# Kernel optimization log

Measured on AMD Instinct MI355X. Metric: run time of the kernel, lower is better.

The kernel has to match this reference:

```python
import jax, jax.numpy as jnp
import numpy as np

MAX_DISPARITY = 192


def _cost_volume(L, R, D):
    """Banded stereo correlation.

    cost[n, j, h, x] = sum_c L[n,c,h,x] * R[n,c,h,x-j], zero when x < j.
    Equivalent to the original full (W,W) matmul followed by per-disparity
    diagonal extraction + left zero-pad, but computed as D shifted
    dot-products (honors the banded structure).
    """
    N, C, H, W = L.shape
    Rp = jnp.pad(R, ((0, 0), (0, 0), (0, 0), (D - 1, 0)))  # left zero-pad

    def step(_, j):
        Rs = jax.lax.dynamic_slice_in_dim(Rp, D - 1 - j, W, axis=3)  # R shifted right by j
        c = jnp.einsum('nchw,nchw->nhw', L, Rs)
        return None, c

    _, cv = jax.lax.scan(step, None, jnp.arange(D))  # (D, N, H, W)
    return jnp.transpose(cv, (1, 0, 2, 3))  # (N, D, H, W)


def setup_inputs() -> dict:
    key = jax.random.key(0)
    ks = jax.random.split(key, 6)
    shapes = [(1, 32, 256, 512), (1, 32, 128, 256), (1, 32, 64, 128)]
    inp = {}
    for i, s in enumerate(shapes):
        inp[f'left{i}'] = jax.random.normal(ks[2 * i], s, dtype=jnp.float32)
        inp[f'right{i}'] = jax.random.normal(ks[2 * i + 1], s, dtype=jnp.float32)
    return inp


def reference(left0, right0, left1, right1, left2, right2):
    lefts = [left0, left1, left2]
    rights = [right0, right1, right2]
    max_disparity = min(MAX_DISPARITY, lefts[0].shape[-1])
    cost_volumes = []
    for i, (L, R) in enumerate(zip(lefts, rights)):
        D = max_disparity // (2 ** i)
        cost_volumes.append(_cost_volume(L, R, D))
    return tuple(cost_volumes)
```

## Files before the change

kernel.cpp:

```cpp
#include <hip/hip_runtime.h>


#define TX 128
#define TJ 192
#define JT 24
#define NCS 8
#define NSTG 4
#define LSW 128
#define RSW 320

#define NBLK_TOTAL 1344

typedef float vf4 __attribute__((ext_vector_type(4)));

__device__ __forceinline__ void gload_lds16(const float* g, float* l)
{
    __builtin_amdgcn_global_load_lds(
        (const __attribute__((address_space(1))) void*)g,
        (__attribute__((address_space(3))) void*)l,
        16, 0, 0);
}

__global__ __launch_bounds__(256, 3)
void cost_volume_fused(const float* __restrict__ L0, const float* __restrict__ R0,
                       const float* __restrict__ L1, const float* __restrict__ R1,
                       const float* __restrict__ L2, const float* __restrict__ R2,
                       float* __restrict__ out)
{
    __shared__ float Ls[2][NCS * LSW];
    __shared__ float Rs[2][NCS * RSW];

    const int id = blockIdx.x;
    const float* L; const float* R; float* o;
    int H, W, D, bx, h;
    if (id < 1024) {
        L = L0; R = R0; o = out;
        H = 256; W = 512; D = 192;
        bx = id & 3; h = id >> 2;
    } else if (id < 1280) {
        int r = id - 1024;
        L = L1; R = R1; o = out + (size_t)192 * 256 * 512;
        H = 128; W = 256; D = 96;
        bx = r & 1; h = r >> 1;
    } else {
        int r = id - 1280;
        L = L2; R = R2; o = out + (size_t)192 * 256 * 512 + (size_t)96 * 128 * 256;
        H = 64; W = 128; D = 48;
        bx = 0; h = r;
    }

    const int x0 = bx * TX;
    const int t  = threadIdx.x;
    const int tx = t & 31;
    const int ty = t >> 5;
    const int jbase = ty * JT;
    const int xg = x0 + 4 * tx;

    const size_t HW = (size_t)H * W;
    const float* Lb = L + (size_t)h * W;
    const float* Rb = R + (size_t)h * W;

    const bool active = (jbase < D);
    const bool live   = active && (xg + 3 >= jbase);

    float acc[JT][4];
    #pragma unroll
    for (int jj = 0; jj < JT; ++jj) {
        acc[jj][0] = 0.f; acc[jj][1] = 0.f; acc[jj][2] = 0.f; acc[jj][3] = 0.f;
    }

    const int rbase = 4 * tx - JT * ty + (TJ - 24);

    auto stage = [&](int c0, int p) {
        {
            int c = t >> 5, q = t & 31;
            gload_lds16(Lb + (size_t)(c0 + c) * HW + x0 + 4 * q, &Ls[p][4 * t]);
        }
        #pragma unroll
        for (int k = 0; k < 3; ++k) {
            int f = t + k * 256;
            if (f < NCS * 80) {
                int c = f / 80, q = f - 80 * c;
                int g = x0 - TJ + 4 * q;
                if (g < 0) g = 0;
                gload_lds16(Rb + (size_t)(c0 + c) * HW + g, &Rs[p][4 * f]);
            }
        }
    };

    stage(0, 0);
    __syncthreads();

    #pragma unroll
    for (int s = 0; s < NSTG; ++s) {
        if (s + 1 < NSTG) stage((s + 1) * NCS, (s + 1) & 1);
        if (live) {
            const float* Lsb = Ls[s & 1];
            const float* Rsb = Rs[s & 1];
            #pragma unroll 1
            for (int c = 0; c < NCS; ++c) {
                const float* Lc = Lsb + c * LSW;
                const float* Rc = Rsb + c * RSW + rbase;
                float lv[4], rw[28];
                *(vf4*)&lv[0] = *(const vf4*)(Lc + 4 * tx);
                #pragma unroll
                for (int k = 0; k < 7; ++k)
                    *(vf4*)&rw[4 * k] = *(const vf4*)(Rc + 4 * k);
                #pragma unroll
                for (int jj = 0; jj < JT; ++jj)
                    #pragma unroll
                    for (int i = 0; i < 4; ++i)
                        acc[jj][i] = fmaf(lv[i], rw[24 + i - jj], acc[jj][i]);
            }
        }
        if (s + 1 < NSTG) __syncthreads();
    }

    if (active) {
        #pragma unroll
        for (int jj = 0; jj < JT; ++jj) {
            int j = jbase + jj;
            float* p = o + ((size_t)j * H + h) * W + xg;
            vf4 v;
            #pragma unroll
            for (int i = 0; i < 4; ++i)
                v[i] = (xg + i >= j) ? acc[jj][i] : 0.f;
            __builtin_nontemporal_store(v, (vf4*)p);
        }
    }
}

extern "C" void kernel_launch(void* const* d_in, const int* in_sizes, int n_in,
                              void* d_out, int out_size, void* d_ws, size_t ws_size,
                              hipStream_t stream)
{
    const float* L0 = (const float*)d_in[0];
    const float* R0 = (const float*)d_in[1];
    const float* L1 = (const float*)d_in[2];
    const float* R1 = (const float*)d_in[3];
    const float* L2 = (const float*)d_in[4];
    const float* R2 = (const float*)d_in[5];
    float* out = (float*)d_out;

    cost_volume_fused<<<dim3(NBLK_TOTAL), dim3(256), 0, stream>>>(
        L0, R0, L1, R1, L2, R2, out);
}
```

Measured before the change: 173.1 us.

## Compute banded correlation with fp16 MFMA tiles and LDS diagonal extraction

```diff
diff --git a/kernel.cpp b/kernel.cpp
--- a/kernel.cpp
+++ b/kernel.cpp
@@ -1,25 +1,12 @@
 #include <hip/hip_runtime.h>
 
-
-#define TX 128
-#define TJ 192
-#define JT 24
-#define NCS 8
-#define NSTG 4
-#define LSW 128
-#define RSW 320
 
 #define NBLK_TOTAL 1344
 
 typedef float vf4 __attribute__((ext_vector_type(4)));
-
-__device__ __forceinline__ void gload_lds16(const float* g, float* l)
-{
-    __builtin_amdgcn_global_load_lds(
-        (const __attribute__((address_space(1))) void*)g,
-        (__attribute__((address_space(3))) void*)l,
-        16, 0, 0);
-}
+typedef float f32x4 __attribute__((ext_vector_type(4)));
+typedef _Float16 h4 __attribute__((ext_vector_type(4)));
+typedef _Float16 h8 __attribute__((ext_vector_type(8)));
 
 __global__ __launch_bounds__(256, 3)
 void cost_volume_fused(const float* __restrict__ L0, const float* __restrict__ R0,
@@ -27,8 +14,8 @@
                        const float* __restrict__ L2, const float* __restrict__ R2,
                        float* __restrict__ out)
 {
-    __shared__ float Ls[2][NCS * LSW];
-    __shared__ float Rs[2][NCS * RSW];
+    __shared__ __align__(16) unsigned short St[448 * 32];
+    __shared__ __align__(16) float Ep[4 * 1024];
 
     const int id = blockIdx.x;
     const float* L; const float* R; float* o;
@@ -49,83 +36,125 @@
         bx = 0; h = r;
     }
 
-    const int x0 = bx * TX;
+    const int x0 = bx * 128;
     const int t  = threadIdx.x;
-    const int tx = t & 31;
-    const int ty = t >> 5;
-    const int jbase = ty * JT;
-    const int xg = x0 + 4 * tx;
+    const int l  = t & 63;
+    const int w_ = t >> 6;
 
     const size_t HW = (size_t)H * W;
     const float* Lb = L + (size_t)h * W;
     const float* Rb = R + (size_t)h * W;
 
-    const bool active = (jbase < D);
-    const bool live   = active && (xg + 3 >= jbase);
+    char* Sb = (char*)St;
 
-    float acc[JT][4];
+    {
+        const int c0 = (t >> 5) * 4;
+        const int x4 = t & 31;
+        const float* gp = Lb + (size_t)c0 * HW + x0 + 4 * x4;
+        vf4 v0 = *(const vf4*)(gp);
+        vf4 v1 = *(const vf4*)(gp + HW);
+        vf4 v2 = *(const vf4*)(gp + 2 * HW);
+        vf4 v3 = *(const vf4*)(gp + 3 * HW);
+        #pragma unroll
+        for (int xi = 0; xi < 4; ++xi) {
+            int row = 4 * x4 + xi;
+            h4 hv = { (_Float16)v0[xi], (_Float16)v1[xi],
+                      (_Float16)v2[xi], (_Float16)v3[xi] };
+            *(h4*)(Sb + row * 64 + ((((c0 >> 3) ^ ((row >> 1) & 3)) << 4)
+                                    | ((c0 & 7) << 1))) = hv;
+        }
+    }
     #pragma unroll
-    for (int jj = 0; jj < JT; ++jj) {
-        acc[jj][0] = 0.f; acc[jj][1] = 0.f; acc[jj][2] = 0.f; acc[jj][3] = 0.f;
+    for (int k = 0; k < 3; ++k) {
+        int idm = t + k * 256;
+        if (idm < 640) {
+            int c0 = (idm / 80) * 4;
+            int x4 = idm - (idm / 80) * 80;
+            int g = x0 - 192 + 4 * x4;
+            vf4 v0 = (vf4)(0.f), v1 = (vf4)(0.f), v2 = (vf4)(0.f), v3 = (vf4)(0.f);
+            if (g >= 0) {
+                const float* gp = Rb + (size_t)c0 * HW + g;
+                v0 = *(const vf4*)(gp);
+                v1 = *(const vf4*)(gp + HW);
+                v2 = *(const vf4*)(gp + 2 * HW);
+                v3 = *(const vf4*)(gp + 3 * HW);
+            }
+            #pragma unroll
+            for (int xi = 0; xi < 4; ++xi) {
+                int row = 128 + 4 * x4 + xi;
+                h4 hv = { (_Float16)v0[xi], (_Float16)v1[xi],
+                          (_Float16)v2[xi], (_Float16)v3[xi] };
+                *(h4*)(Sb + row * 64 + ((((c0 >> 3) ^ ((row >> 1) & 3)) << 4)
+                                        | ((c0 & 7) << 1))) = hv;
+            }
+        }
+    }
+    __syncthreads();
+
+    const int lm = l & 15;
+    const int kg = l >> 4;
+    const int q0 = 2 * w_;
+
+    f32x4 acc0[13], acc1[13];
+    #pragma unroll
+    for (int i = 0; i < 13; ++i) { acc0[i] = (f32x4)(0.f); acc1[i] = (f32x4)(0.f); }
+
+    const int rowA0 = 16 * q0 + lm;
+    const int rowA1 = rowA0 + 16;
+    h8 a0 = *(const h8*)(Sb + rowA0 * 64 + ((kg ^ ((rowA0 >> 1) & 3)) << 4));
+    h8 a1 = *(const h8*)(Sb + rowA1 * 64 + ((kg ^ ((rowA1 >> 1) & 3)) << 4));
+
+    #pragma unroll
+    for (int nt = 0; nt <= 13; ++nt) {
+        int rowB = 128 + 16 * (q0 + nt) + lm;
+        h8 b = *(const h8*)(Sb + rowB * 64 + ((kg ^ ((rowB >> 1) & 3)) << 4));
+        if (nt <= 12)
+            acc0[nt] = __builtin_amdgcn_mfma_f32_16x16x32_f16(a0, b, acc0[nt], 0, 0, 0);
+        if (nt >= 1)
+            acc1[nt - 1] = __builtin_amdgcn_mfma_f32_16x16x32_f16(a1, b, acc1[nt - 1], 0, 0, 0);
     }
 
-    const int rbase = 4 * tx - JT * ty + (TJ - 24);
+    float* Cw = Ep + w_ * 1024;
+    const int Dg = D >> 4;
 
-    auto stage = [&](int c0, int p) {
+    #pragma unroll
+    for (int jg = 0; jg < 12; ++jg) {
+        if (jg >= Dg) break;
         {
-            int c = t >> 5, q = t & 31;
-            gload_lds16(Lb + (size_t)(c0 + c) * HW + x0 + 4 * q, &Ls[p][4 * t]);
+            #pragma unroll
+            for (int e = 0; e < 2; ++e) {
+                int rel = (e == 0) ? (11 - jg) : 12;
+                if (e == 1 && jg != 0) break;
+                f32x4 ta = acc0[rel];
+                f32x4 tb = acc1[rel];
+                float* b0 = Cw + (0 * 2 + (rel & 1)) * 256;
+                float* b1 = Cw + (1 * 2 + (rel & 1)) * 256;
+                #pragma unroll
+                for (int rr = 0; rr < 4; ++rr) {
+                    int m = kg * 4 + rr;
+                    int off = m * 16 + (lm ^ ((m >> 2) << 2));
+                    b0[off] = ta[rr];
+                    b1[off] = tb[rr];
+                }
+            }
         }
         #pragma unroll
-        for (int k = 0; k < 3; ++k) {
-            int f = t + k * 256;
-            if (f < NCS * 80) {
-                int c = f / 80, q = f - 80 * c;
-                int g = x0 - TJ + 4 * q;
-                if (g < 0) g = 0;
-                gload_lds16(Rb + (size_t)(c0 + c) * HW + g, &Rs[p][4 * f]);
+        for (int r = 0; r < 2; ++r) {
+            int j  = 16 * jg + 8 * r + (l >> 3);
+            int xbl = (l & 7) * 4;
+            int mt = xbl >> 4;
+            f32x4 v;
+            #pragma unroll
+            for (int i = 0; i < 4; ++i) {
+                int xl = xbl + i;
+                int m = xl & 15;
+                int xp = 32 * w_ + xl + 192 - j;
+                int rel = (xp >> 4) - (q0 + mt);
+                int n = xp & 15;
+                v[i] = Cw[(mt * 2 + (rel & 1)) * 256 + m * 16 + (n ^ ((m >> 2) << 2))];
             }
-        }
-    };
-
-    stage(0, 0);
-    __syncthreads();
-
-    #pragma unroll
-    for (int s = 0; s < NSTG; ++s) {
-        if (s + 1 < NSTG) stage((s + 1) * NCS, (s + 1) & 1);
-        if (live) {
-            const float* Lsb = Ls[s & 1];
-            const float* Rsb = Rs[s & 1];
-            #pragma unroll 1
-            for (int c = 0; c < NCS; ++c) {
-                const float* Lc = Lsb + c * LSW;
-                const float* Rc = Rsb + c * RSW + rbase;
-                float lv[4], rw[28];
-                *(vf4*)&lv[0] = *(const vf4*)(Lc + 4 * tx);
-                #pragma unroll
-                for (int k = 0; k < 7; ++k)
-                    *(vf4*)&rw[4 * k] = *(const vf4*)(Rc + 4 * k);
-                #pragma unroll
-                for (int jj = 0; jj < JT; ++jj)
-                    #pragma unroll
-                    for (int i = 0; i < 4; ++i)
-                        acc[jj][i] = fmaf(lv[i], rw[24 + i - jj], acc[jj][i]);
-            }
-        }
-        if (s + 1 < NSTG) __syncthreads();
-    }
-
-    if (active) {
-        #pragma unroll
-        for (int jj = 0; jj < JT; ++jj) {
-            int j = jbase + jj;
-            float* p = o + ((size_t)j * H + h) * W + xg;
-            vf4 v;
-            #pragma unroll
-            for (int i = 0; i < 4; ++i)
-                v[i] = (xg + i >= j) ? acc[jj][i] : 0.f;
-            __builtin_nontemporal_store(v, (vf4*)p);
+            float* p = o + ((size_t)j * H + h) * W + x0 + 32 * w_ + xbl;
+            __builtin_nontemporal_store(*(vf4*)&v, (vf4*)p);
         }
     }
 }
```

New measurement: 217.5 us. +25.7%, slower.
